# Kernel optimization log

Hardware: AMD Instinct MI355X
Metric: run time of the kernel (lower is better)

## Reference

```python
import jax, jax.numpy as jnp
import numpy as np

N_NODES = 100000
N_EDGES = 1600000
IN_C, HID_C, OUT_C = 128, 128, 40
BN_EPS = 1e-5


def gcn_conv(x, W, b, edge_index, n):
    # PyG GCNConv: h = x @ W, add self-loops, symmetric normalization, scatter-add to targets, + bias
    h = x @ W  # [N, C_out]
    loops = jnp.arange(n, dtype=edge_index.dtype)
    src = jnp.concatenate([edge_index[0], loops])  # messages flow source -> target
    dst = jnp.concatenate([edge_index[1], loops])
    deg = jax.ops.segment_sum(jnp.ones_like(dst, dtype=h.dtype), dst, num_segments=n)
    dinv = jnp.where(deg > 0, jax.lax.rsqrt(deg), 0.0).astype(h.dtype)
    norm = dinv[src] * dinv[dst]  # [E+N]
    msg = h[src] * norm[:, None]
    out = jax.ops.segment_sum(msg, dst, num_segments=n)
    return out + b


def batch_norm(x, gamma, beta):
    # training-mode batchnorm over the node dimension (biased variance, as torch)
    mean = jnp.mean(x, axis=0)
    var = jnp.mean(jnp.square(x - mean), axis=0)
    return (x - mean) * jax.lax.rsqrt(var + BN_EPS) * gamma + beta


def setup_inputs() -> dict:
    key = jax.random.key(0)
    ks = jax.random.split(key, 8)
    x = jax.random.normal(ks[0], (N_NODES, IN_C), dtype=jnp.float32)
    edge_index = jax.random.randint(ks[1], (2, N_EDGES), 0, N_NODES, dtype=jnp.int64)
    def glorot(k, fi, fo):
        s = np.sqrt(6.0 / (fi + fo)).astype(np.float32)
        return jax.random.uniform(k, (fi, fo), jnp.float32, -s, s)
    return {
        "x": x,
        "edge_index": edge_index,
        "W1": glorot(ks[2], IN_C, HID_C), "b1": jnp.zeros((HID_C,), jnp.float32),
        "g1": jnp.ones((HID_C,), jnp.float32), "bt1": jnp.zeros((HID_C,), jnp.float32),
        "W2": glorot(ks[3], HID_C, HID_C), "b2": jnp.zeros((HID_C,), jnp.float32),
        "g2": jnp.ones((HID_C,), jnp.float32), "bt2": jnp.zeros((HID_C,), jnp.float32),
        "W3": glorot(ks[4], HID_C, OUT_C), "b3": jnp.zeros((OUT_C,), jnp.float32),
    }


def reference(x, edge_index, W1, b1, g1, bt1, W2, b2, g2, bt2, W3, b3):
    n = x.shape[0]
    # layer 1: GCNConv -> BatchNorm -> ReLU (dropout p=0.0 / eval -> identity)
    h = gcn_conv(x, W1, b1, edge_index, n)
    h = jax.nn.relu(batch_norm(h, g1, bt1))
    # layer 2
    h = gcn_conv(h, W2, b2, edge_index, n)
    h = jax.nn.relu(batch_norm(h, g2, bt2))
    # output layer (no norm/act)
    return gcn_conv(h, W3, b3, edge_index, n)
```

## Files before the change

kernel.cpp:

```cpp
#include <hip/hip_runtime.h>
#include <hip/hip_fp16.h>
#include <cstdint>

#define BN_EPS 1e-5f
#define PCHUNK 4096
#define BCAP 16384
#define CSRCAP 16384

typedef _Float16 f16;
typedef _Float16 f16x8 __attribute__((ext_vector_type(8)));
typedef _Float16 f16x4 __attribute__((ext_vector_type(4)));
typedef float f32x4 __attribute__((ext_vector_type(4)));


__device__ __forceinline__ void load_edge(const void* eb, int E, bool w64,
                                          int e, int& s, int& d) {
  if (w64) {
    const long long* p = (const long long*)eb;
    s = (int)p[e];
    d = (int)p[E + e];
  } else {
    const int* p = (const int*)eb;
    s = p[e];
    d = p[E + e];
  }
}

__global__ __launch_bounds__(512) void part_k(const void* __restrict__ eb, int E,
                                              int* __restrict__ pcur,
                                              int2* __restrict__ part) {
  __shared__ int hist[256], lofs[256], gbase[256], lcur[256];
  __shared__ int sa[256], sb[256];
  __shared__ int2 stage[PCHUNK];
  __shared__ int w64f;
  const int t = threadIdx.x;
  const int e0 = blockIdx.x * PCHUNK;
  const int cnt = min(PCHUNK, E - e0);
  if (t < 256) hist[t] = 0;
  if (t == 0) w64f = 0;
  __syncthreads();
  {
    const unsigned* w = (const unsigned*)eb;
    int nz = 0;
    int cov = min(cnt, 512);
    for (int k = t; k < cov; k += 512) nz |= (w[2 * (size_t)(e0 + k) + 1] != 0u);
    if (nz) atomicOr(&w64f, 1);
  }
  __syncthreads();
  const bool w64 = (w64f == 0);
  int2 ed[8];
#pragma unroll
  for (int k = 0; k < 8; k++) {
    int idx = t + k * 512;
    if (idx < cnt) {
      int s, d;
      load_edge(eb, E, w64, e0 + idx, s, d);
      ed[k].x = s;
      ed[k].y = d;
      atomicAdd(&hist[d >> 9], 1);
    }
  }
  __syncthreads();
  if (t < 256) sa[t] = hist[t];
  __syncthreads();
  int* src = sa;
  int* dst = sb;
  for (int off = 1; off < 256; off <<= 1) {
    int val = 0;
    if (t < 256) val = src[t] + (t >= off ? src[t - off] : 0);
    __syncthreads();
    if (t < 256) dst[t] = val;
    __syncthreads();
    int* tmp = src; src = dst; dst = tmp;
  }
  int c = 0;
  if (t < 256) {
    c = hist[t];
    lofs[t] = src[t] - c;
    int cpad = (c + 7) & ~7;
    gbase[t] = (c > 0) ? (t * BCAP + atomicAdd(&pcur[t], cpad)) : 0;
    lcur[t] = src[t] - c;
  }
  __syncthreads();
#pragma unroll
  for (int k = 0; k < 8; k++) {
    int idx = t + k * 512;
    if (idx < cnt) {
      int b = ed[k].y >> 9;
      int p = atomicAdd(&lcur[b], 1);
      stage[p] = ed[k];
    }
  }
  __syncthreads();
  for (int idx = t; idx < cnt; idx += 512) {
    int2 e = stage[idx];
    int b = e.y >> 9;
    part[gbase[b] + (idx - lofs[b])] = e;
  }
  if (t < 256 && c > 0) {
    int cpad = (c + 7) & ~7;
    for (int k = c; k < cpad; k++) part[gbase[t] + k] = make_int2(0, -1);
  }
}

__global__ __launch_bounds__(512) void sort_k(const int2* __restrict__ part,
                                              const int* __restrict__ pcur,
                                              int2* __restrict__ rpc,
                                              float* __restrict__ dinv,
                                              int* __restrict__ csr, int n) {
  __shared__ int lhist[512], lcur[512], lstart[512];
  __shared__ int sa[512], sb[512];
  const int b = blockIdx.x;
  const int d0 = b << 9;
  const int t = threadIdx.x;
  const int nloc = min(512, n - d0);
  lhist[t] = 0;
  __syncthreads();
  const int base = b * BCAP;
  const int T = pcur[b];
  for (int idx = t; idx < T; idx += 512) {
    int2 e = part[base + idx];
    if (e.y >= 0) atomicAdd(&lhist[e.y - d0], 1);
  }
  __syncthreads();
  int c = lhist[t];
  int cpad = (c + 7) & ~7;
  sa[t] = cpad;
  __syncthreads();
  int* src = sa;
  int* dst = sb;
  for (int off = 1; off < 512; off <<= 1) {
    int val = src[t] + (t >= off ? src[t - off] : 0);
    __syncthreads();
    dst[t] = val;
    __syncthreads();
    int* tmp = src; src = dst; dst = tmp;
  }
  int start = b * CSRCAP + src[t] - cpad;
  if (t < nloc) {
    rpc[d0 + t] = make_int2(start, cpad);
    dinv[d0 + t] = rsqrtf((float)(c + 1));
  }
  lstart[t] = start;
  lcur[t] = start;
  __syncthreads();
  for (int idx = t; idx < T; idx += 512) {
    int2 e = part[base + idx];
    if (e.y >= 0) {
      int pos = atomicAdd(&lcur[e.y - d0], 1);
      csr[pos] = e.x;
    }
  }
  if (t < nloc) {
    for (int k = c; k < cpad; k++) csr[lstart[t] + k] = n;
  }
}

__global__ void prep_all(const float* __restrict__ W1, const float* __restrict__ W2,
                         const float* __restrict__ W3, f16* __restrict__ Wt1,
                         f16* __restrict__ Wt2, f16* __restrict__ Wt3) {
  int b = blockIdx.x, k = threadIdx.x;
  if (b < 128) {
    Wt1[(size_t)b * 128 + k] = (f16)W1[(size_t)k * 128 + b];
  } else if (b < 256) {
    int nc = b - 128;
    Wt2[(size_t)nc * 128 + k] = (f16)W2[(size_t)k * 128 + nc];
  } else {
    int nc = b - 256;
    Wt3[(size_t)nc * 128 + k] = (nc < 40) ? (f16)W3[(size_t)k * 40 + nc] : (f16)0.f;
  }
}

template <int NCP, bool BN, bool F32IN>
__global__ __launch_bounds__(256) void gemm_mfma(const void* __restrict__ Xv,
                                                 const f16* __restrict__ Wt,
                                                 const float* __restrict__ bn_acc,
                                                 const float* __restrict__ g,
                                                 const float* __restrict__ bt,
                                                 float inv_n,
                                                 const float* __restrict__ dinv,
                                                 f16* __restrict__ H, int n) {
  constexpr int CB = NCP / 16;
  __shared__ f16 Xs[128][136];
  __shared__ f16 Ws[NCP][136];
  __shared__ float bnS[128], bnH[128];
  const int t = threadIdx.x;
  const int m0 = blockIdx.x * 128;

  if (BN) {
    if (t < 128) {
      float mean = bn_acc[t] * inv_n;
      float var = bn_acc[128 + t] * inv_n - mean * mean;
      float sc = g[t] * rsqrtf(var + BN_EPS);
      bnS[t] = sc;
      bnH[t] = fmaf(-mean, sc, bt[t]);
    }
    __syncthreads();
  }

  if constexpr (F32IN) {
    const float* X = (const float*)Xv;
#pragma unroll
    for (int p = 0; p < 16; p++) {
      int idx = p * 256 + t;
      int row = idx >> 5, c = (idx & 31) * 4;
      float4 v = make_float4(0.f, 0.f, 0.f, 0.f);
      if (m0 + row < n) v = *(const float4*)&X[(size_t)(m0 + row) * 128 + c];
      if (BN) {
        v.x = fmaxf(fmaf(v.x, bnS[c + 0], bnH[c + 0]), 0.f);
        v.y = fmaxf(fmaf(v.y, bnS[c + 1], bnH[c + 1]), 0.f);
        v.z = fmaxf(fmaf(v.z, bnS[c + 2], bnH[c + 2]), 0.f);
        v.w = fmaxf(fmaf(v.w, bnS[c + 3], bnH[c + 3]), 0.f);
      }
      f16x4 h = {(f16)v.x, (f16)v.y, (f16)v.z, (f16)v.w};
      *(f16x4*)&Xs[row][c] = h;
    }
  } else {
    const f16* X = (const f16*)Xv;
#pragma unroll
    for (int p = 0; p < 8; p++) {
      int idx = p * 256 + t;
      int row = idx >> 4, c = (idx & 15) * 8;
      f16x8 v = {0, 0, 0, 0, 0, 0, 0, 0};
      if (m0 + row < n) v = *(const f16x8*)&X[(size_t)(m0 + row) * 128 + c];
      if (BN) {
#pragma unroll
        for (int j = 0; j < 8; j++) {
          float f = (float)v[j];
          f = fmaxf(fmaf(f, bnS[c + j], bnH[c + j]), 0.f);
          v[j] = (f16)f;
        }
      }
      *(f16x8*)&Xs[row][c] = v;
    }
  }
#pragma unroll
  for (int idx = t; idx < NCP * 16; idx += 256) {
    int row = idx >> 4, c = (idx & 15) * 8;
    *(f16x8*)&Ws[row][c] = *(const f16x8*)&Wt[(size_t)row * 128 + c];
  }
  __syncthreads();

  const int w = t >> 6, l = t & 63;
  const int lr = l & 15, lq = l >> 4;
  f32x4 acc[2][CB];
#pragma unroll
  for (int i = 0; i < 2; i++)
#pragma unroll
    for (int j = 0; j < CB; j++) acc[i][j] = (f32x4){0.f, 0.f, 0.f, 0.f};

#pragma unroll
  for (int kb = 0; kb < 4; kb++) {
    f16x8 xf0 = *(const f16x8*)&Xs[w * 32 + lr][kb * 32 + lq * 8];
    f16x8 xf1 = *(const f16x8*)&Xs[w * 32 + 16 + lr][kb * 32 + lq * 8];
#pragma unroll
    for (int cb = 0; cb < CB; cb++) {
      f16x8 wf = *(const f16x8*)&Ws[cb * 16 + lr][kb * 32 + lq * 8];
      acc[0][cb] = __builtin_amdgcn_mfma_f32_16x16x32_f16(wf, xf0, acc[0][cb], 0, 0, 0);
      acc[1][cb] = __builtin_amdgcn_mfma_f32_16x16x32_f16(wf, xf1, acc[1][cb], 0, 0, 0);
    }
  }
#pragma unroll
  for (int rg = 0; rg < 2; rg++) {
    int row = m0 + w * 32 + rg * 16 + lr;
    if (row > n) continue;
    float dv = (row < n) ? dinv[row] : 0.f;
#pragma unroll
    for (int cb = 0; cb < CB; cb++) {
      int col = cb * 16 + lq * 4;
      f32x4 a = acc[rg][cb];
      f16x4 h = {(f16)(a[0] * dv), (f16)(a[1] * dv), (f16)(a[2] * dv),
                 (f16)(a[3] * dv)};
      *(f16x4*)&H[(size_t)row * NCP + col] = h;
    }
  }
}

__global__ __launch_bounds__(256) void agg128h(const f16* __restrict__ H,
                                               const int2* __restrict__ rpc,
                                               const int* __restrict__ csr,
                                               const float* __restrict__ dinv,
                                               const float* __restrict__ bias,
                                               f16* __restrict__ out, int n) {
  const int lane = threadIdx.x & 63;
  const int sub = lane >> 4, cl = lane & 15;
  const int q = (blockIdx.x * 256 + threadIdx.x) >> 6;
  const int i = q * 4 + sub;
  const bool valid = (i < n);
  const int ic = valid ? i : 0;
  f16x8 a = *(const f16x8*)&H[(size_t)ic * 128 + cl * 8];
  int2 rc = rpc[ic];
  const int e0 = rc.x, cntp = rc.y;
  for (int j = 0; j < cntp; j += 8) {
    int4 c0 = *(const int4*)&csr[e0 + j];
    int4 c1 = *(const int4*)&csr[e0 + j + 4];
    f16x8 v0 = *(const f16x8*)&H[(size_t)c0.x * 128 + cl * 8];
    f16x8 v1 = *(const f16x8*)&H[(size_t)c0.y * 128 + cl * 8];
    f16x8 v2 = *(const f16x8*)&H[(size_t)c0.z * 128 + cl * 8];
    f16x8 v3 = *(const f16x8*)&H[(size_t)c0.w * 128 + cl * 8];
    f16x8 v4 = *(const f16x8*)&H[(size_t)c1.x * 128 + cl * 8];
    f16x8 v5 = *(const f16x8*)&H[(size_t)c1.y * 128 + cl * 8];
    f16x8 v6 = *(const f16x8*)&H[(size_t)c1.z * 128 + cl * 8];
    f16x8 v7 = *(const f16x8*)&H[(size_t)c1.w * 128 + cl * 8];
    f16x8 t01 = v0 + v1;
    f16x8 t23 = v2 + v3;
    f16x8 t45 = v4 + v5;
    f16x8 t67 = v6 + v7;
    a = a + ((t01 + t23) + (t45 + t67));
  }
  if (valid) {
    float dv = dinv[ic];
    float4 b0 = *(const float4*)&bias[cl * 8];
    float4 b1 = *(const float4*)&bias[cl * 8 + 4];
    f16x8 h;
    h[0] = (f16)fmaf((float)a[0], dv, b0.x);
    h[1] = (f16)fmaf((float)a[1], dv, b0.y);
    h[2] = (f16)fmaf((float)a[2], dv, b0.z);
    h[3] = (f16)fmaf((float)a[3], dv, b0.w);
    h[4] = (f16)fmaf((float)a[4], dv, b1.x);
    h[5] = (f16)fmaf((float)a[5], dv, b1.y);
    h[6] = (f16)fmaf((float)a[6], dv, b1.z);
    h[7] = (f16)fmaf((float)a[7], dv, b1.w);
    *(f16x8*)&out[(size_t)i * 128 + cl * 8] = h;
  }
}

__global__ __launch_bounds__(256) void agg64h(const f16* __restrict__ H,
                                              const int2* __restrict__ rpc,
                                              const int* __restrict__ csr,
                                              const float* __restrict__ dinv,
                                              const float* __restrict__ bias,
                                              float* __restrict__ out, int n) {
  const int lane = threadIdx.x & 63;
  const int sub = lane >> 4, cl = lane & 15;
  const int q = (blockIdx.x * 256 + threadIdx.x) >> 6;
  const int i = q * 4 + sub;
  const bool valid = (i < n);
  const int ic = valid ? i : 0;
  f16x4 a = *(const f16x4*)&H[(size_t)ic * 64 + cl * 4];
  int2 rc = rpc[ic];
  const int e0 = rc.x, cntp = rc.y;
  for (int j = 0; j < cntp; j += 8) {
    int4 c0 = *(const int4*)&csr[e0 + j];
    int4 c1 = *(const int4*)&csr[e0 + j + 4];
    f16x4 v0 = *(const f16x4*)&H[(size_t)c0.x * 64 + cl * 4];
    f16x4 v1 = *(const f16x4*)&H[(size_t)c0.y * 64 + cl * 4];
    f16x4 v2 = *(const f16x4*)&H[(size_t)c0.z * 64 + cl * 4];
    f16x4 v3 = *(const f16x4*)&H[(size_t)c0.w * 64 + cl * 4];
    f16x4 v4 = *(const f16x4*)&H[(size_t)c1.x * 64 + cl * 4];
    f16x4 v5 = *(const f16x4*)&H[(size_t)c1.y * 64 + cl * 4];
    f16x4 v6 = *(const f16x4*)&H[(size_t)c1.z * 64 + cl * 4];
    f16x4 v7 = *(const f16x4*)&H[(size_t)c1.w * 64 + cl * 4];
    f16x4 t01 = v0 + v1;
    f16x4 t23 = v2 + v3;
    f16x4 t45 = v4 + v5;
    f16x4 t67 = v6 + v7;
    a = a + ((t01 + t23) + (t45 + t67));
  }
  if (valid && cl < 10) {
    float dv = dinv[ic];
    float4 bb = *(const float4*)&bias[cl * 4];
    float4 o;
    o.x = fmaf((float)a[0], dv, bb.x);
    o.y = fmaf((float)a[1], dv, bb.y);
    o.z = fmaf((float)a[2], dv, bb.z);
    o.w = fmaf((float)a[3], dv, bb.w);
    *(float4*)&out[(size_t)i * 40 + cl * 4] = o;
  }
}

__global__ __launch_bounds__(256) void bn_stats_h(const f16* __restrict__ H, int n,
                                                  float* __restrict__ acc) {
  int t = threadIdx.x;
  int c2 = t & 63;
  int rg = t >> 6;
  float2 s = {0.f, 0.f}, s2 = {0.f, 0.f};
  for (int r = blockIdx.x * 4 + rg; r < n; r += gridDim.x * 4) {
    float2 v = __half22float2(*(const __half2*)&H[(size_t)r * 128 + c2 * 2]);
    s.x += v.x;
    s.y += v.y;
    s2.x = fmaf(v.x, v.x, s2.x);
    s2.y = fmaf(v.y, v.y, s2.y);
  }
  __shared__ float ls[4][128], ls2[4][128];
  ls[rg][c2 * 2] = s.x;
  ls[rg][c2 * 2 + 1] = s.y;
  ls2[rg][c2 * 2] = s2.x;
  ls2[rg][c2 * 2 + 1] = s2.y;
  __syncthreads();
  if (t < 128) {
    float a_ = ls[0][t] + ls[1][t] + ls[2][t] + ls[3][t];
    float b_ = ls2[0][t] + ls2[1][t] + ls2[2][t] + ls2[3][t];
    atomicAdd(&acc[t], a_);
    atomicAdd(&acc[128 + t], b_);
  }
}

extern "C" void kernel_launch(void* const* d_in, const int* in_sizes, int n_in,
                              void* d_out, int out_size, void* d_ws, size_t ws_size,
                              hipStream_t stream) {
  const float* x = (const float*)d_in[0];
  const void* eb = d_in[1];
  const float* W1 = (const float*)d_in[2];
  const float* b1 = (const float*)d_in[3];
  const float* g1 = (const float*)d_in[4];
  const float* bt1 = (const float*)d_in[5];
  const float* W2 = (const float*)d_in[6];
  const float* b2 = (const float*)d_in[7];
  const float* g2 = (const float*)d_in[8];
  const float* bt2 = (const float*)d_in[9];
  const float* W3 = (const float*)d_in[10];
  const float* b3 = (const float*)d_in[11];

  const int n = in_sizes[0] / 128;
  const int E = in_sizes[1] / 2;
  const float inv_n = 1.0f / (float)n;

  char* w = (char*)d_ws;
  auto alloc = [&](size_t bytes) {
    void* p = (void*)w;
    w += (bytes + 255) & ~(size_t)255;
    return p;
  };
  const int NBKT = (n + 511) / 512;
  f16* hA = (f16*)alloc((size_t)(n + 1) * 128 * 2);
  f16* hB = (f16*)alloc((size_t)(n + 1) * 128 * 2);
  int* csr = (int*)alloc((size_t)NBKT * CSRCAP * 4);
  int2* part = (int2*)alloc((size_t)NBKT * BCAP * 8);
  float* dinv = (float*)alloc((size_t)n * 4);
  int2* rpc = (int2*)alloc((size_t)n * 8);
  f16* Wt1 = (f16*)alloc(128 * 128 * 2);
  f16* Wt2 = (f16*)alloc(128 * 128 * 2);
  f16* Wt3 = (f16*)alloc(64 * 128 * 2);
  int* pcur = (int*)alloc(256 * 4);
  float* bn_acc1 = (float*)alloc(256 * 4);
  float* bn_acc2 = (float*)alloc(256 * 4);
  size_t zbytes = (char*)bn_acc2 + 256 * 4 - (char*)pcur;
  hipMemsetAsync(pcur, 0, zbytes, stream);

  const int PB = (E + PCHUNK - 1) / PCHUNK;

  prep_all<<<320, 128, 0, stream>>>(W1, W2, W3, Wt1, Wt2, Wt3);

  part_k<<<PB, 512, 0, stream>>>(eb, E, pcur, part);
  sort_k<<<NBKT, 512, 0, stream>>>(part, pcur, rpc, dinv, csr, n);

  const int GB = (n + 128) / 128;
  const int NQ = (n + 3) / 4;
  const int AGB = (NQ + 3) / 4;

  gemm_mfma<128, false, true><<<GB, 256, 0, stream>>>(x, Wt1, nullptr, nullptr,
                                                      nullptr, inv_n, dinv, hA, n);
  agg128h<<<AGB, 256, 0, stream>>>(hA, rpc, csr, dinv, b1, hB, n);
  bn_stats_h<<<1024, 256, 0, stream>>>(hB, n, bn_acc1);
  gemm_mfma<128, true, false><<<GB, 256, 0, stream>>>(hB, Wt2, bn_acc1, g1, bt1,
                                                      inv_n, dinv, hA, n);
  agg128h<<<AGB, 256, 0, stream>>>(hA, rpc, csr, dinv, b2, hB, n);
  bn_stats_h<<<1024, 256, 0, stream>>>(hB, n, bn_acc2);
  gemm_mfma<64, true, false><<<GB, 256, 0, stream>>>(hB, Wt3, bn_acc2, g2, bt2,
                                                     inv_n, dinv, hA, n);
  agg64h<<<AGB, 256, 0, stream>>>(hA, rpc, csr, dinv, b3, (float*)d_out, n);
}
```

Before: 422.2 us.

## Fuse batchnorm statistics into aggregation kernel and enlarge edge partition chunk

The separate bn_stats pass is removed. Each aggregation block now reduces per-column sum and sum-of-squares in fp32 through wave shuffles and shared-memory atomics, then adds them to one of four global accumulator copies, which the next GEMM sums before computing mean and variance. This avoids two full reads of the hidden activations and two kernel launches, at the cost of more atomics and an extra block barrier in the aggregation. Separately, the edge partition chunk doubles to 8192 with 16 staged edges per thread, which halves the number of partition blocks but raises register and LDS use. The statistics are now taken from fp32 values before the fp16 store rather than from the stored fp16 values.

Result: faster. 374.3 us (-11.3%).

```diff
diff --git a/kernel.cpp b/kernel.cpp
--- a/kernel.cpp
+++ b/kernel.cpp
@@ -3,7 +3,7 @@
 #include <cstdint>
 
 #define BN_EPS 1e-5f
-#define PCHUNK 4096
+#define PCHUNK 8192
 #define BCAP 16384
 #define CSRCAP 16384
 
@@ -48,9 +48,9 @@
   }
   __syncthreads();
   const bool w64 = (w64f == 0);
-  int2 ed[8];
-#pragma unroll
-  for (int k = 0; k < 8; k++) {
+  int2 ed[16];
+#pragma unroll
+  for (int k = 0; k < 16; k++) {
     int idx = t + k * 512;
     if (idx < cnt) {
       int s, d;
@@ -83,7 +83,7 @@
   }
   __syncthreads();
 #pragma unroll
-  for (int k = 0; k < 8; k++) {
+  for (int k = 0; k < 16; k++) {
     int idx = t + k * 512;
     if (idx < cnt) {
       int b = ed[k].y >> 9;
@@ -189,8 +189,11 @@
 
   if (BN) {
     if (t < 128) {
-      float mean = bn_acc[t] * inv_n;
-      float var = bn_acc[128 + t] * inv_n - mean * mean;
+      float s0 = bn_acc[t] + bn_acc[256 + t] + bn_acc[512 + t] + bn_acc[768 + t];
+      float s1 = bn_acc[128 + t] + bn_acc[384 + t] + bn_acc[640 + t] +
+                 bn_acc[896 + t];
+      float mean = s0 * inv_n;
+      float var = s1 * inv_n - mean * mean;
       float sc = g[t] * rsqrtf(var + BN_EPS);
       bnS[t] = sc;
       bnH[t] = fmaf(-mean, sc, bt[t]);
@@ -281,10 +284,18 @@
                                                const int* __restrict__ csr,
                                                const float* __restrict__ dinv,
                                                const float* __restrict__ bias,
-                                               f16* __restrict__ out, int n) {
-  const int lane = threadIdx.x & 63;
+                                               f16* __restrict__ out,
+                                               float* __restrict__ bnacc, int n) {
+  __shared__ float lsum[128], lsq[128];
+  const int t = threadIdx.x;
+  if (t < 128) {
+    lsum[t] = 0.f;
+    lsq[t] = 0.f;
+  }
+  __syncthreads();
+  const int lane = t & 63;
   const int sub = lane >> 4, cl = lane & 15;
-  const int q = (blockIdx.x * 256 + threadIdx.x) >> 6;
+  const int q = (blockIdx.x * 256 + t) >> 6;
   const int i = q * 4 + sub;
   const bool valid = (i < n);
   const int ic = valid ? i : 0;
@@ -308,20 +319,50 @@
     f16x8 t67 = v6 + v7;
     a = a + ((t01 + t23) + (t45 + t67));
   }
+  float dv = dinv[ic];
+  float4 b0 = *(const float4*)&bias[cl * 8];
+  float4 b1 = *(const float4*)&bias[cl * 8 + 4];
+  float ov[8];
+  ov[0] = fmaf((float)a[0], dv, b0.x);
+  ov[1] = fmaf((float)a[1], dv, b0.y);
+  ov[2] = fmaf((float)a[2], dv, b0.z);
+  ov[3] = fmaf((float)a[3], dv, b0.w);
+  ov[4] = fmaf((float)a[4], dv, b1.x);
+  ov[5] = fmaf((float)a[5], dv, b1.y);
+  ov[6] = fmaf((float)a[6], dv, b1.z);
+  ov[7] = fmaf((float)a[7], dv, b1.w);
   if (valid) {
-    float dv = dinv[ic];
-    float4 b0 = *(const float4*)&bias[cl * 8];
-    float4 b1 = *(const float4*)&bias[cl * 8 + 4];
     f16x8 h;
-    h[0] = (f16)fmaf((float)a[0], dv, b0.x);
-    h[1] = (f16)fmaf((float)a[1], dv, b0.y);
-    h[2] = (f16)fmaf((float)a[2], dv, b0.z);
-    h[3] = (f16)fmaf((float)a[3], dv, b0.w);
-    h[4] = (f16)fmaf((float)a[4], dv, b1.x);
-    h[5] = (f16)fmaf((float)a[5], dv, b1.y);
-    h[6] = (f16)fmaf((float)a[6], dv, b1.z);
-    h[7] = (f16)fmaf((float)a[7], dv, b1.w);
+#pragma unroll
+    for (int c = 0; c < 8; c++) h[c] = (f16)ov[c];
     *(f16x8*)&out[(size_t)i * 128 + cl * 8] = h;
+  }
+  float hs[8], qs[8];
+#pragma unroll
+  for (int c = 0; c < 8; c++) {
+    float v = valid ? ov[c] : 0.f;
+    hs[c] = v;
+    qs[c] = v * v;
+  }
+#pragma unroll
+  for (int c = 0; c < 8; c++) {
+    hs[c] += __shfl_xor(hs[c], 16);
+    hs[c] += __shfl_xor(hs[c], 32);
+    qs[c] += __shfl_xor(qs[c], 16);
+    qs[c] += __shfl_xor(qs[c], 32);
+  }
+  if (sub == 0) {
+#pragma unroll
+    for (int c = 0; c < 8; c++) {
+      atomicAdd(&lsum[cl * 8 + c], hs[c]);
+      atomicAdd(&lsq[cl * 8 + c], qs[c]);
+    }
+  }
+  __syncthreads();
+  if (t < 128) {
+    float* dstp = bnacc + (blockIdx.x & 3) * 256;
+    atomicAdd(&dstp[t], lsum[t]);
+    atomicAdd(&dstp[128 + t], lsq[t]);
   }
 }
 
@@ -369,33 +410,6 @@
   }
 }
 
-__global__ __launch_bounds__(256) void bn_stats_h(const f16* __restrict__ H, int n,
-                                                  float* __restrict__ acc) {
-  int t = threadIdx.x;
-  int c2 = t & 63;
-  int rg = t >> 6;
-  float2 s = {0.f, 0.f}, s2 = {0.f, 0.f};
-  for (int r = blockIdx.x * 4 + rg; r < n; r += gridDim.x * 4) {
-    float2 v = __half22float2(*(const __half2*)&H[(size_t)r * 128 + c2 * 2]);
-    s.x += v.x;
-    s.y += v.y;
-    s2.x = fmaf(v.x, v.x, s2.x);
-    s2.y = fmaf(v.y, v.y, s2.y);
-  }
-  __shared__ float ls[4][128], ls2[4][128];
-  ls[rg][c2 * 2] = s.x;
-  ls[rg][c2 * 2 + 1] = s.y;
-  ls2[rg][c2 * 2] = s2.x;
-  ls2[rg][c2 * 2 + 1] = s2.y;
-  __syncthreads();
-  if (t < 128) {
-    float a_ = ls[0][t] + ls[1][t] + ls[2][t] + ls[3][t];
-    float b_ = ls2[0][t] + ls2[1][t] + ls2[2][t] + ls2[3][t];
-    atomicAdd(&acc[t], a_);
-    atomicAdd(&acc[128 + t], b_);
-  }
-}
-
 extern "C" void kernel_launch(void* const* d_in, const int* in_sizes, int n_in,
                               void* d_out, int out_size, void* d_ws, size_t ws_size,
                               hipStream_t stream) {
@@ -433,9 +447,9 @@
   f16* Wt2 = (f16*)alloc(128 * 128 * 2);
   f16* Wt3 = (f16*)alloc(64 * 128 * 2);
   int* pcur = (int*)alloc(256 * 4);
-  float* bn_acc1 = (float*)alloc(256 * 4);
-  float* bn_acc2 = (float*)alloc(256 * 4);
-  size_t zbytes = (char*)bn_acc2 + 256 * 4 - (char*)pcur;
+  float* bn_acc1 = (float*)alloc(1024 * 4);
+  float* bn_acc2 = (float*)alloc(1024 * 4);
+  size_t zbytes = (char*)bn_acc2 + 1024 * 4 - (char*)pcur;
   hipMemsetAsync(pcur, 0, zbytes, stream);
 
   const int PB = (E + PCHUNK - 1) / PCHUNK;
@@ -451,12 +465,10 @@
 
   gemm_mfma<128, false, true><<<GB, 256, 0, stream>>>(x, Wt1, nullptr, nullptr,
                                                       nullptr, inv_n, dinv, hA, n);
-  agg128h<<<AGB, 256, 0, stream>>>(hA, rpc, csr, dinv, b1, hB, n);
-  bn_stats_h<<<1024, 256, 0, stream>>>(hB, n, bn_acc1);
+  agg128h<<<AGB, 256, 0, stream>>>(hA, rpc, csr, dinv, b1, hB, bn_acc1, n);
   gemm_mfma<128, true, false><<<GB, 256, 0, stream>>>(hB, Wt2, bn_acc1, g1, bt1,
                                                       inv_n, dinv, hA, n);
-  agg128h<<<AGB, 256, 0, stream>>>(hA, rpc, csr, dinv, b2, hB, n);
-  bn_stats_h<<<1024, 256, 0, stream>>>(hB, n, bn_acc2);
+  agg128h<<<AGB, 256, 0, stream>>>(hA, rpc, csr, dinv, b2, hB, bn_acc2, n);
   gemm_mfma<64, true, false><<<GB, 256, 0, stream>>>(hB, Wt3, bn_acc2, g2, bt2,
                                                      inv_n, dinv, hA, n);
   agg64h<<<AGB, 256, 0, stream>>>(hA, rpc, csr, dinv, b3, (float*)d_out, n);
```
